# Kernel tuning notes

Hardware: AMD Instinct MI355X
Metric: run time of the kernel (lower is better)

## Reference

```python
import jax, jax.numpy as jnp
import numpy as np

B, K, NV, H, T = 4, 2, 32, 16, 4096
G = K * NV                 # conv groups = 64
OPG = 2 * (NV + H)         # out channels per group = 96 (instantaneous doubles channels)
TEMPERATURE = 1.0


def setup_inputs() -> dict:
    key = jax.random.key(0)
    k1, k2, k3 = jax.random.split(key, 3)
    x = jax.random.normal(k1, (B, G * H, T), dtype=jnp.float32)
    W = jax.random.normal(k2, (G, OPG, H), dtype=jnp.float32) * (1.0 / np.sqrt(H))
    b = jax.random.normal(k3, (G, OPG), dtype=jnp.float32) * 0.01
    return {"x": x, "W": W, "b": b}


def reference(x, W, b):
    # pad one zero step at end of sequence (ConstantPad1d((0,1),0))
    xp = jnp.pad(x, ((0, 0), (0, 0), (0, 1)))            # (B, G*H, T+1)
    xg = xp.reshape(B, G, H, T + 1)
    # TCN modeled as grouped pointwise conv: per-group linear over channel dim
    y = jnp.einsum('bgdt,god->bgot', xg, W) + b[None, :, :, None]  # (B, G, OPG, T+1)
    # split temporal / instantaneous branches with the causal shift
    y = y.reshape(B * K, NV, 2, NV + H, T + 1)
    xt = y[:, :, 0, :, :-1]                               # (B*K, NV, NV+H, T)
    xi = y[:, :, 1, :, 1:]                                # (B*K, NV, NV+H, T)
    # split attention logits (first NV channels) and context (last H channels)
    ctx = jnp.concatenate([xt[:, :, NV:, :], xi[:, :, NV:, :]], axis=1)   # (B*K, 2*NV, H, T)
    att = jnp.concatenate([xt[:, :, :NV, :], xi[:, :, :NV, :]], axis=2)   # (B*K, NV, 2*NV, T)
    att = jax.nn.softmax(att / TEMPERATURE, axis=2)
    out = jnp.einsum('bijt,bjdt->bidt', att, ctx)         # (B*K, NV, H, T)
    out = out.reshape(B, K * NV * H, T)
    attn = att.reshape(B, K, NV, 2 * NV, T)
    return out, attn
```

## Files before the change

### kernel.cpp

```cpp
#include <hip/hip_runtime.h>
#include <stdint.h>

#define T_  4096
#define GS  296
#define US  16
#define AJ  652
#define AT  40
#define CJ  260

static __device__ __forceinline__ float bflo(uint32_t w){ union{uint32_t u;float f;}v; v.u=w<<16; return v.f; }
static __device__ __forceinline__ float bfhi(uint32_t w){ union{uint32_t u;float f;}v; v.u=w&0xFFFF0000u; return v.f; }
static __device__ __forceinline__ float bf2f(uint16_t u){ union{uint32_t u;float f;}v; v.u=((uint32_t)u)<<16; return v.f; }
static __device__ __forceinline__ uint16_t f2bf(float f){
    union{float f;uint32_t u;}v; v.f=f; uint32_t x=v.u;
    return (uint16_t)((x + 0x7FFFu + ((x>>16)&1u)) >> 16);
}

__global__ __launch_bounds__(1024, 4)
void tamcad_kernel(const float* __restrict__ x, const float* __restrict__ W,
                   const float* __restrict__ bias, float* __restrict__ out)
{
    __shared__ float    xsr[32*GS];
    __shared__ uint16_t As [64*AJ];
    __shared__ uint16_t Cs [64*CJ];

    const int tid   = threadIdx.x;
    const int bk    = blockIdx.x >> 5;
    const int chunk = blockIdx.x & 31;
    const int b     = bk >> 1;
    const int k     = bk & 1;

    const int oq   = tid & 31;
    const int g    = tid >> 5;
    const int slot = oq >> 4;

    const int dl = tid & 15;
    const int gl = (tid >> 4) & 31;
    const int hl = tid >> 9;

    float wreg[3][16], breg[3];
    int   aoff[3], coff[3];
    bool  isl[3];
    #pragma unroll
    for (int r = 0; r < 3; ++r) {
        const int o = oq*3 + r;
        const float4* wp = reinterpret_cast<const float4*>(W + (((size_t)(k*32+g))*96 + o)*16);
        float4 w0=wp[0], w1=wp[1], w2=wp[2], w3=wp[3];
        wreg[r][ 0]=w0.x; wreg[r][ 1]=w0.y; wreg[r][ 2]=w0.z; wreg[r][ 3]=w0.w;
        wreg[r][ 4]=w1.x; wreg[r][ 5]=w1.y; wreg[r][ 6]=w1.z; wreg[r][ 7]=w1.w;
        wreg[r][ 8]=w2.x; wreg[r][ 9]=w2.y; wreg[r][10]=w2.z; wreg[r][11]=w2.w;
        wreg[r][12]=w3.x; wreg[r][13]=w3.y; wreg[r][14]=w3.z; wreg[r][15]=w3.w;
        breg[r] = bias[(k*32+g)*96 + o];
        if (o < 32)      { isl[r]=true;  aoff[r]=o*AJ + g;            coff[r]=0; }
        else if (o < 48) { isl[r]=false; coff[r]=g*CJ + (o-32);       aoff[r]=0; }
        else if (o < 80) { isl[r]=true;  aoff[r]=(o-16)*AJ + g;       coff[r]=0; }
        else             { isl[r]=false; coff[r]=(32+g)*CJ + (o-80);  aoff[r]=0; }
    }

    const float* xrow = x + ((size_t)b*1024 + (size_t)(k*32+gl)*16 + dl) * (size_t)T_;

    float4 pA, pB; float pS = 0.0f;
    {
        const float* gp = xrow + chunk*128 + hl*8;
        pA = *(const float4*)(gp + 0);
        pB = *(const float4*)(gp + 4);
        pS = (hl && (chunk*128 + 16) < T_) ? gp[8] : 0.0f;
    }

    for (int l = 0; l < 8; ++l) {
        const int t0 = chunk*128 + l*16;

        {
            float* xp = xsr + gl*GS + dl;
            const int ub = hl*8;
            xp[(ub+0)*US]=pA.x; xp[(ub+1)*US]=pA.y; xp[(ub+2)*US]=pA.z; xp[(ub+3)*US]=pA.w;
            xp[(ub+4)*US]=pB.x; xp[(ub+5)*US]=pB.y; xp[(ub+6)*US]=pB.z; xp[(ub+7)*US]=pB.w;
            if (hl) xp[16*US] = pS;
        }
        __syncthreads();

        if (l < 7) {
            const int t0n = t0 + 16;
            const float* gp = xrow + t0n + hl*8;
            pA = *(const float4*)(gp + 0);
            pB = *(const float4*)(gp + 4);
            pS = (hl && (t0n + 16) < T_) ? gp[8] : 0.0f;
        }

        {
            float xv[16];
            {
                const float4* p4 = reinterpret_cast<const float4*>(xsr + g*GS + slot*US);
                float4 A0=p4[0], A1=p4[1], A2=p4[2], A3=p4[3];
                xv[ 0]=A0.x; xv[ 1]=A0.y; xv[ 2]=A0.z; xv[ 3]=A0.w;
                xv[ 4]=A1.x; xv[ 5]=A1.y; xv[ 6]=A1.z; xv[ 7]=A1.w;
                xv[ 8]=A2.x; xv[ 9]=A2.y; xv[10]=A2.z; xv[11]=A2.w;
                xv[12]=A3.x; xv[13]=A3.y; xv[14]=A3.z; xv[15]=A3.w;
            }
            for (int tp = 0; tp < 16; ++tp) {
                float yv[3];
                #pragma unroll
                for (int r = 0; r < 3; ++r) {
                    float a = breg[r];
                    #pragma unroll
                    for (int d = 0; d < 16; ++d) a = fmaf(wreg[r][d], xv[d], a);
                    yv[r] = a;
                }
                {
                    const float4* p4 = reinterpret_cast<const float4*>(xsr + g*GS + (tp+1+slot)*US);
                    float4 A0=p4[0], A1=p4[1], A2=p4[2], A3=p4[3];
                    xv[ 0]=A0.x; xv[ 1]=A0.y; xv[ 2]=A0.z; xv[ 3]=A0.w;
                    xv[ 4]=A1.x; xv[ 5]=A1.y; xv[ 6]=A1.z; xv[ 7]=A1.w;
                    xv[ 8]=A2.x; xv[ 9]=A2.y; xv[10]=A2.z; xv[11]=A2.w;
                    xv[12]=A3.x; xv[13]=A3.y; xv[14]=A3.z; xv[15]=A3.w;
                }
                float ev[3];
                float ssum = 0.0f;
                #pragma unroll
                for (int r = 0; r < 3; ++r) {
                    ev[r] = 0.0f;
                    if (isl[r]) { ev[r] = __expf(yv[r]); ssum += ev[r]; }
                }
                #pragma unroll
                for (int s = 1; s < 32; s <<= 1) ssum += __shfl_xor(ssum, s);
                const float rinv = __builtin_amdgcn_rcpf(ssum);
                #pragma unroll
                for (int r = 0; r < 3; ++r) {
                    if (isl[r]) As[aoff[r] + tp*AT] = f2bf(ev[r] * rinv);
                    else        Cs[coff[r] + tp*16] = f2bf(yv[r]);
                }
            }
        }
        __syncthreads();

        {
            const int t  = tid >> 6;
            const int r6 = tid & 63;
            const int i0 = (r6 & 7) << 2;
            const int d0 = (r6 >> 3) << 1;
            float acc[4][2];
            #pragma unroll
            for (int ii = 0; ii < 4; ++ii) { acc[ii][0]=0.f; acc[ii][1]=0.f; }
            const uint16_t* Ap = As + t*AT + i0;
            const uint16_t* Cp = Cs + t*16 + d0;
            #pragma unroll 8
            for (int j = 0; j < 64; ++j) {
                uint2    aw = *(const uint2*)(Ap + j*AJ);
                uint32_t cw = *(const uint32_t*)(Cp + j*CJ);
                float a0=bflo(aw.x), a1=bfhi(aw.x), a2=bflo(aw.y), a3=bfhi(aw.y);
                float c0=bflo(cw),   c1=bfhi(cw);
                acc[0][0]=fmaf(a0,c0,acc[0][0]); acc[0][1]=fmaf(a0,c1,acc[0][1]);
                acc[1][0]=fmaf(a1,c0,acc[1][0]); acc[1][1]=fmaf(a1,c1,acc[1][1]);
                acc[2][0]=fmaf(a2,c0,acc[2][0]); acc[2][1]=fmaf(a2,c1,acc[2][1]);
                acc[3][0]=fmaf(a3,c0,acc[3][0]); acc[3][1]=fmaf(a3,c1,acc[3][1]);
            }
            const int skew = (r6 & 7) * 4;
            #pragma unroll
            for (int ii = 0; ii < 4; ++ii)
                #pragma unroll
                for (int dd = 0; dd < 2; ++dd) {
                    const int row = (i0+ii)*16 + d0+dd;
                    xsr[row*17 + skew + t] = acc[ii][dd];
                }
        }
        __syncthreads();

        {
            if (tid < 512) {
                const int skew = (tid >> 6) * 4;
                float ov[16];
                #pragma unroll
                for (int u = 0; u < 16; ++u) ov[u] = xsr[tid*17 + skew + u];
                float* op = out + ((size_t)b*1024 + k*512 + tid)*(size_t)T_ + t0;
                *(float4*)(op + 0)  = make_float4(ov[ 0],ov[ 1],ov[ 2],ov[ 3]);
                *(float4*)(op + 4)  = make_float4(ov[ 4],ov[ 5],ov[ 6],ov[ 7]);
                *(float4*)(op + 8)  = make_float4(ov[ 8],ov[ 9],ov[10],ov[11]);
                *(float4*)(op + 12) = make_float4(ov[12],ov[13],ov[14],ov[15]);
            }
            float* attn_base = out + (size_t)4*1024*(size_t)T_;
            #pragma unroll
            for (int rr = 0; rr < 2; ++rr) {
                const int q = tid + 1024*rr;
                const int i = q >> 6;
                const int j = q & 63;
                const uint16_t* ap = As + j*AJ + i;
                float av[16];
                #pragma unroll
                for (int u = 0; u < 16; ++u) av[u] = bf2f(ap[u*AT]);
                float* tp2 = attn_base + (((size_t)bk*32 + i)*64 + j)*(size_t)T_ + t0;
                *(float4*)(tp2 + 0)  = make_float4(av[ 0],av[ 1],av[ 2],av[ 3]);
                *(float4*)(tp2 + 4)  = make_float4(av[ 4],av[ 5],av[ 6],av[ 7]);
                *(float4*)(tp2 + 8)  = make_float4(av[ 8],av[ 9],av[10],av[11]);
                *(float4*)(tp2 + 12) = make_float4(av[12],av[13],av[14],av[15]);
            }
        }
        __syncthreads();
    }
}

extern "C" void kernel_launch(void* const* d_in, const int* in_sizes, int n_in,
                              void* d_out, int out_size, void* d_ws, size_t ws_size,
                              hipStream_t stream) {
    const float* x  = (const float*)d_in[0];
    const float* W  = (const float*)d_in[1];
    const float* bs = (const float*)d_in[2];
    float* out = (float*)d_out;
    tamcad_kernel<<<dim3(256), dim3(1024), 0, stream>>>(x, W, bs, out);
}
```

Baseline: 239.5 us.

## Batch softmax shuffle reductions and split output/attn stores across thread halves

The projection+softmax loop now processes eight timesteps at a time, computing all exps first and then doing the cross-lane sum reductions for eight values in one interleaved pass, which gives more independent shuffles to hide latency. Exps are computed for all outputs, including context channels. The store phase gives the output writes to threads 0-511 and the attention writes to threads 512-1023. Attention reads now use 64-bit LDS loads covering four i-rows per thread, instead of every thread doing two rounds of scalar 16-bit loads. Register pressure rises from holding eight timesteps of exp values.

```diff
diff --git a/kernel.cpp b/kernel.cpp
--- a/kernel.cpp
+++ b/kernel.cpp
@@ -10,7 +10,6 @@
 
 static __device__ __forceinline__ float bflo(uint32_t w){ union{uint32_t u;float f;}v; v.u=w<<16; return v.f; }
 static __device__ __forceinline__ float bfhi(uint32_t w){ union{uint32_t u;float f;}v; v.u=w&0xFFFF0000u; return v.f; }
-static __device__ __forceinline__ float bf2f(uint16_t u){ union{uint32_t u;float f;}v; v.u=((uint32_t)u)<<16; return v.f; }
 static __device__ __forceinline__ uint16_t f2bf(float f){
     union{float f;uint32_t u;}v; v.f=f; uint32_t x=v.u;
     return (uint16_t)((x + 0x7FFFu + ((x>>16)&1u)) >> 16);
@@ -39,8 +38,7 @@
     const int hl = tid >> 9;
 
     float wreg[3][16], breg[3];
-    int   aoff[3], coff[3];
-    bool  isl[3];
+    int aoff[3], coff[3]; bool isl[3];
     #pragma unroll
     for (int r = 0; r < 3; ++r) {
         const int o = oq*3 + r;
@@ -87,48 +85,47 @@
             pS = (hl && (t0n + 16) < T_) ? gp[8] : 0.0f;
         }
 
-        {
-            float xv[16];
-            {
-                const float4* p4 = reinterpret_cast<const float4*>(xsr + g*GS + slot*US);
-                float4 A0=p4[0], A1=p4[1], A2=p4[2], A3=p4[3];
-                xv[ 0]=A0.x; xv[ 1]=A0.y; xv[ 2]=A0.z; xv[ 3]=A0.w;
-                xv[ 4]=A1.x; xv[ 5]=A1.y; xv[ 6]=A1.z; xv[ 7]=A1.w;
-                xv[ 8]=A2.x; xv[ 9]=A2.y; xv[10]=A2.z; xv[11]=A2.w;
-                xv[12]=A3.x; xv[13]=A3.y; xv[14]=A3.z; xv[15]=A3.w;
-            }
-            for (int tp = 0; tp < 16; ++tp) {
-                float yv[3];
-                #pragma unroll
-                for (int r = 0; r < 3; ++r) {
-                    float a = breg[r];
-                    #pragma unroll
-                    for (int d = 0; d < 16; ++d) a = fmaf(wreg[r][d], xv[d], a);
-                    yv[r] = a;
-                }
+        #pragma unroll
+        for (int th = 0; th < 2; ++th) {
+            float ev0[8], ev1[8], ev2[8], asum[8];
+            #pragma unroll
+            for (int q = 0; q < 8; ++q) {
+                const int tp = th*8 + q;
+                float xv[16];
                 {
-                    const float4* p4 = reinterpret_cast<const float4*>(xsr + g*GS + (tp+1+slot)*US);
+                    const float4* p4 = reinterpret_cast<const float4*>(xsr + g*GS + (tp+slot)*US);
                     float4 A0=p4[0], A1=p4[1], A2=p4[2], A3=p4[3];
                     xv[ 0]=A0.x; xv[ 1]=A0.y; xv[ 2]=A0.z; xv[ 3]=A0.w;
                     xv[ 4]=A1.x; xv[ 5]=A1.y; xv[ 6]=A1.z; xv[ 7]=A1.w;
                     xv[ 8]=A2.x; xv[ 9]=A2.y; xv[10]=A2.z; xv[11]=A2.w;
                     xv[12]=A3.x; xv[13]=A3.y; xv[14]=A3.z; xv[15]=A3.w;
                 }
-                float ev[3];
-                float ssum = 0.0f;
-                #pragma unroll
-                for (int r = 0; r < 3; ++r) {
-                    ev[r] = 0.0f;
-                    if (isl[r]) { ev[r] = __expf(yv[r]); ssum += ev[r]; }
-                }
-                #pragma unroll
-                for (int s = 1; s < 32; s <<= 1) ssum += __shfl_xor(ssum, s);
-                const float rinv = __builtin_amdgcn_rcpf(ssum);
-                #pragma unroll
-                for (int r = 0; r < 3; ++r) {
-                    if (isl[r]) As[aoff[r] + tp*AT] = f2bf(ev[r] * rinv);
-                    else        Cs[coff[r] + tp*16] = f2bf(yv[r]);
-                }
+                float y0 = breg[0], y1 = breg[1], y2 = breg[2];
+                #pragma unroll
+                for (int d = 0; d < 16; ++d) {
+                    y0 = fmaf(wreg[0][d], xv[d], y0);
+                    y1 = fmaf(wreg[1][d], xv[d], y1);
+                    y2 = fmaf(wreg[2][d], xv[d], y2);
+                }
+                const float e0 = __expf(y0), e1 = __expf(y1), e2 = __expf(y2);
+                asum[q] = (isl[0]?e0:0.f) + (isl[1]?e1:0.f) + (isl[2]?e2:0.f);
+                if (!isl[0]) Cs[coff[0] + tp*16] = f2bf(y0);
+                if (!isl[1]) Cs[coff[1] + tp*16] = f2bf(y1);
+                if (!isl[2]) Cs[coff[2] + tp*16] = f2bf(y2);
+                ev0[q]=e0; ev1[q]=e1; ev2[q]=e2;
+            }
+            #pragma unroll
+            for (int s = 1; s < 32; s <<= 1) {
+                #pragma unroll
+                for (int q = 0; q < 8; ++q) asum[q] += __shfl_xor(asum[q], s);
+            }
+            #pragma unroll
+            for (int q = 0; q < 8; ++q) {
+                const int tp = th*8 + q;
+                const float rinv = __builtin_amdgcn_rcpf(asum[q]);
+                if (isl[0]) As[aoff[0] + tp*AT] = f2bf(ev0[q]*rinv);
+                if (isl[1]) As[aoff[1] + tp*AT] = f2bf(ev1[q]*rinv);
+                if (isl[2]) As[aoff[2] + tp*AT] = f2bf(ev2[q]*rinv);
             }
         }
         __syncthreads();
@@ -154,7 +151,7 @@
                 acc[2][0]=fmaf(a2,c0,acc[2][0]); acc[2][1]=fmaf(a2,c1,acc[2][1]);
                 acc[3][0]=fmaf(a3,c0,acc[3][0]); acc[3][1]=fmaf(a3,c1,acc[3][1]);
             }
-            const int skew = (r6 & 7) * 4;
+            const int skew = i0;
             #pragma unroll
             for (int ii = 0; ii < 4; ++ii)
                 #pragma unroll
@@ -165,33 +162,36 @@
         }
         __syncthreads();
 
-        {
-            if (tid < 512) {
-                const int skew = (tid >> 6) * 4;
-                float ov[16];
-                #pragma unroll
-                for (int u = 0; u < 16; ++u) ov[u] = xsr[tid*17 + skew + u];
-                float* op = out + ((size_t)b*1024 + k*512 + tid)*(size_t)T_ + t0;
-                *(float4*)(op + 0)  = make_float4(ov[ 0],ov[ 1],ov[ 2],ov[ 3]);
-                *(float4*)(op + 4)  = make_float4(ov[ 4],ov[ 5],ov[ 6],ov[ 7]);
-                *(float4*)(op + 8)  = make_float4(ov[ 8],ov[ 9],ov[10],ov[11]);
-                *(float4*)(op + 12) = make_float4(ov[12],ov[13],ov[14],ov[15]);
-            }
+        if (tid < 512) {
+            const int skew = (tid >> 6) * 4;
+            float ov[16];
+            #pragma unroll
+            for (int u = 0; u < 16; ++u) ov[u] = xsr[tid*17 + skew + u];
+            float* op = out + ((size_t)b*1024 + k*512 + tid)*(size_t)T_ + t0;
+            *(float4*)(op + 0)  = make_float4(ov[ 0],ov[ 1],ov[ 2],ov[ 3]);
+            *(float4*)(op + 4)  = make_float4(ov[ 4],ov[ 5],ov[ 6],ov[ 7]);
+            *(float4*)(op + 8)  = make_float4(ov[ 8],ov[ 9],ov[10],ov[11]);
+            *(float4*)(op + 12) = make_float4(ov[12],ov[13],ov[14],ov[15]);
+        } else {
+            const int q  = tid - 512;
+            const int j  = q & 63;
+            const int i0 = (q >> 6) << 2;
             float* attn_base = out + (size_t)4*1024*(size_t)T_;
-            #pragma unroll
-            for (int rr = 0; rr < 2; ++rr) {
-                const int q = tid + 1024*rr;
-                const int i = q >> 6;
-                const int j = q & 63;
-                const uint16_t* ap = As + j*AJ + i;
-                float av[16];
-                #pragma unroll
-                for (int u = 0; u < 16; ++u) av[u] = bf2f(ap[u*AT]);
-                float* tp2 = attn_base + (((size_t)bk*32 + i)*64 + j)*(size_t)T_ + t0;
-                *(float4*)(tp2 + 0)  = make_float4(av[ 0],av[ 1],av[ 2],av[ 3]);
-                *(float4*)(tp2 + 4)  = make_float4(av[ 4],av[ 5],av[ 6],av[ 7]);
-                *(float4*)(tp2 + 8)  = make_float4(av[ 8],av[ 9],av[10],av[11]);
-                *(float4*)(tp2 + 12) = make_float4(av[12],av[13],av[14],av[15]);
+            const uint16_t* ap = As + j*AJ + i0;
+            float* tp0 = attn_base + (((size_t)bk*32 + i0)*64 + j)*(size_t)T_ + t0;
+            #pragma unroll
+            for (int c = 0; c < 4; ++c) {
+                float av[4][4];
+                #pragma unroll
+                for (int u = 0; u < 4; ++u) {
+                    uint2 aw = *(const uint2*)(ap + (c*4+u)*AT);
+                    av[0][u]=bflo(aw.x); av[1][u]=bfhi(aw.x);
+                    av[2][u]=bflo(aw.y); av[3][u]=bfhi(aw.y);
+                }
+                #pragma unroll
+                for (int ii = 0; ii < 4; ++ii)
+                    *(float4*)(tp0 + (size_t)ii*64*T_ + c*4) =
+                        make_float4(av[ii][0],av[ii][1],av[ii][2],av[ii][3]);
             }
         }
         __syncthreads();
```

After: 345.9 us. +44.4%, slower.
